# Performance work log

Measured on AMD Instinct MI355X. Metric: run time of the kernel, lower is better.

The kernel has to match this reference:

```python
import jax, jax.numpy as jnp
import numpy as np

B, L, D, H, TOPO = 2, 1024, 1024, 16, 8
Dh = D // H
N_SLOTS = B * L


def _rope_apply(x, cos, sin):
    # x: [B,H,L,Dh]; cos/sin: [B,1,L,Dh//2]
    x1 = x[..., 0::2]
    x2 = x[..., 1::2]
    y1 = x1 * cos - x2 * sin
    y2 = x1 * sin + x2 * cos
    return jnp.stack([y1, y2], axis=-1).reshape(x.shape)


def setup_inputs() -> dict:
    key = jax.random.key(0)
    ks = jax.random.split(key, 6)
    x = jax.random.normal(ks[0], (B, L, D), dtype=jnp.float32)
    topo_active = jax.random.normal(ks[1], (B, L, TOPO), dtype=jnp.float32)
    k_cache = jnp.zeros((1, H, N_SLOTS, Dh), dtype=jnp.float32)
    v_cache = jnp.zeros((1, H, N_SLOTS, Dh), dtype=jnp.float32)
    Wqkv = jax.random.normal(ks[2], (3 * D, D), dtype=jnp.float32) * 0.02
    Wproj = jax.random.normal(ks[3], (D, D), dtype=jnp.float32) * 0.02
    Wfreq = jax.random.normal(ks[4], (Dh // 2, TOPO), dtype=jnp.float32) * 0.02
    # each token (b, pos) writes to physical slot b*L + pos
    slot_mapping = jnp.arange(N_SLOTS, dtype=jnp.int64)
    # paged causal mask: query (b, i) may see slot s iff slot belongs to batch b and pos(s) <= i
    s = jnp.arange(N_SLOTS)
    sb = s // L           # batch owning each slot
    sp = s % L            # position within that sequence
    b_idx = jnp.arange(B)[:, None, None]
    i_idx = jnp.arange(L)[None, :, None]
    block_mask = ((sb[None, None, :] == b_idx) & (sp[None, None, :] <= i_idx))[:, None]  # [B,1,L,S]
    return {"x": x, "topo_active": topo_active, "k_cache": k_cache, "v_cache": v_cache,
            "Wqkv": Wqkv, "Wproj": Wproj, "Wfreq": Wfreq,
            "slot_mapping": slot_mapping, "block_mask": block_mask}


def reference(x, topo_active, k_cache, v_cache, Wqkv, Wproj, Wfreq, slot_mapping, block_mask):
    Bx, Lx, Dx = x.shape
    # qkv projection -> q,k,v [B,H,L,Dh]
    qkv = (x @ Wqkv.T).reshape(Bx, Lx, 3, H, Dh).transpose(2, 0, 3, 1, 4)
    q, k, v = qkv[0], qkv[1], qkv[2]
    # RnRoPE: topo -> per-position frequencies, rotate q and k
    freqs = (topo_active @ Wfreq.T)[:, None]  # [B,1,L,Dh//2]
    cos, sin = jnp.cos(freqs), jnp.sin(freqs)
    q = _rope_apply(q, cos, sin)
    k = _rope_apply(k, cos, sin)
    # commit new k/v into the paged cache via slot_mapping scatter
    k_flat = k.transpose(0, 2, 1, 3).reshape(Bx * Lx, H, Dh).swapaxes(0, 1)  # [H,BL,Dh]
    v_flat = v.transpose(0, 2, 1, 3).reshape(Bx * Lx, H, Dh).swapaxes(0, 1)
    kc = k_cache[0].at[:, slot_mapping].set(k_flat)  # [H,S,Dh]
    vc = v_cache[0].at[:, slot_mapping].set(v_flat)
    # masked (block-sparse) attention over the physical cache
    scale = 1.0 / jnp.sqrt(jnp.float32(Dh))
    scores = jnp.einsum('bhld,hsd->bhls', q, kc) * scale
    scores = jnp.where(block_mask, scores, -jnp.inf)
    p = jax.nn.softmax(scores, axis=-1)
    out = jnp.einsum('bhls,hsd->bhld', p, vc)
    out = out.transpose(0, 2, 1, 3).reshape(Bx, Lx, Dx)
    return out @ Wproj.T
```

## Files before the change

### kernel.cpp

```cpp
#include <hip/hip_runtime.h>
#include <hip/hip_bf16.h>
#include <hip/hip_cooperative_groups.h>
#include <math.h>

namespace cg = cooperative_groups;

#define H_N 16
#define DH 64
#define LSEQ 1024
#define BATCH 2
#define NSLOT 2048
#define DMODEL 1024

typedef __bf16 bf16x8 __attribute__((ext_vector_type(8)));
typedef __bf16 bf16x4 __attribute__((ext_vector_type(4)));
typedef float f32x4 __attribute__((ext_vector_type(4)));

template <int BM, int BN, int BK>
__device__ __forceinline__ void gemm_coreT(const __bf16* __restrict__ A,
                                           const __bf16* __restrict__ Bm,
                                           int K, int m0, int n0,
                                           __bf16* As, __bf16* Bs,
                                           f32x4 acc[BM / 32][BN / 32],
                                           int tid, int wr, int wc, int lane) {
    constexpr int MF = BM / 32, NF = BN / 32;
    constexpr int SLOTS = BK / 8;
    constexpr int RPI = 256 / SLOTS;
    constexpr int AIT = BM / RPI;
    constexpr int BIT = BN / RPI;
    const f32x4 z = {0.f, 0.f, 0.f, 0.f};
#pragma unroll
    for (int m = 0; m < MF; ++m)
#pragma unroll
        for (int n = 0; n < NF; ++n) acc[m][n] = z;

    const int l15 = lane & 15, g = lane >> 4;
    const int wv = tid >> 6;
    const int srow = tid / SLOTS, sslot = tid % SLOTS;
    const int ssrc = (sslot ^ (srow & 7)) * 8;

#pragma unroll
    for (int i = 0; i < AIT; ++i) {
        int row = i * RPI + srow;
        __builtin_amdgcn_global_load_lds(
            (const __attribute__((address_space(1))) void*)(A + (size_t)(m0 + row) * K + ssrc),
            (__attribute__((address_space(3))) void*)(As + i * 2048 + wv * 512), 16, 0, 0);
    }
#pragma unroll
    for (int i = 0; i < BIT; ++i) {
        int row = i * RPI + srow;
        __builtin_amdgcn_global_load_lds(
            (const __attribute__((address_space(1))) void*)(Bm + (size_t)(n0 + row) * K + ssrc),
            (__attribute__((address_space(3))) void*)(Bs + i * 2048 + wv * 512), 16, 0, 0);
    }
    __syncthreads();

    const int NT = K / BK;
    for (int t = 0; t < NT; ++t) {
        const int cur = t & 1;
        __bf16* Ac = As + cur * (BM * BK);
        __bf16* Bc = Bs + cur * (BN * BK);
        if (t + 1 < NT) {
            const int k0 = (t + 1) * BK;
            __bf16* An = As + (1 - cur) * (BM * BK);
            __bf16* Bn = Bs + (1 - cur) * (BN * BK);
#pragma unroll
            for (int i = 0; i < AIT; ++i) {
                int row = i * RPI + srow;
                __builtin_amdgcn_global_load_lds(
                    (const __attribute__((address_space(1))) void*)(A + (size_t)(m0 + row) * K + k0 + ssrc),
                    (__attribute__((address_space(3))) void*)(An + i * 2048 + wv * 512), 16, 0, 0);
            }
#pragma unroll
            for (int i = 0; i < BIT; ++i) {
                int row = i * RPI + srow;
                __builtin_amdgcn_global_load_lds(
                    (const __attribute__((address_space(1))) void*)(Bm + (size_t)(n0 + row) * K + k0 + ssrc),
                    (__attribute__((address_space(3))) void*)(Bn + i * 2048 + wv * 512), 16, 0, 0);
            }
        }
        __builtin_amdgcn_s_setprio(1);
#pragma unroll
        for (int kk = 0; kk < BK / 32; ++kk) {
            const int k16 = kk * 4 + g;
            bf16x8 af[MF], bfr[NF];
#pragma unroll
            for (int m = 0; m < MF; ++m) {
                int row = wr * (BM / 2) + m * 16 + l15;
                int slot = k16 ^ (row & 7);
                af[m] = *reinterpret_cast<const bf16x8*>(Ac + row * BK + slot * 8);
            }
#pragma unroll
            for (int n = 0; n < NF; ++n) {
                int col = wc * (BN / 2) + n * 16 + l15;
                int slot = k16 ^ (col & 7);
                bfr[n] = *reinterpret_cast<const bf16x8*>(Bc + col * BK + slot * 8);
            }
#pragma unroll
            for (int m = 0; m < MF; ++m)
#pragma unroll
                for (int n = 0; n < NF; ++n)
                    acc[m][n] = __builtin_amdgcn_mfma_f32_16x16x32_bf16(af[m], bfr[n], acc[m][n], 0, 0, 0);
        }
        __builtin_amdgcn_s_setprio(0);
        __syncthreads();
    }
}

__device__ __forceinline__ void setup_body(int blk, int tid,
                                           const float* x, const float* Wqkv, const float* Wproj,
                                           const float* topo, const float* Wfreq,
                                           __bf16* xb, __bf16* Wqkvb, __bf16* Wprojb,
                                           float* cosb, float* sinb) {
    if (blk < 6144) {
        const float* in;
        __bf16* ob;
        int base;
        if (blk < 2048)      { in = x;     ob = xb;     base = blk; }
        else if (blk < 5120) { in = Wqkv;  ob = Wqkvb;  base = blk - 2048; }
        else                 { in = Wproj; ob = Wprojb; base = blk - 5120; }
        int i = (base * 256 + tid) * 4;
        float4 v = *reinterpret_cast<const float4*>(in + i);
        struct B4 { __bf16 a, b, c, d; };
        B4 o{(__bf16)v.x, (__bf16)v.y, (__bf16)v.z, (__bf16)v.w};
        *reinterpret_cast<B4*>(ob + i) = o;
    } else {
        int s = (blk - 6144) * 8 + (tid >> 5);
        int j = tid & 31;
        float f = 0.f;
#pragma unroll
        for (int t = 0; t < 8; ++t) f += topo[s * 8 + t] * Wfreq[j * 8 + t];
        cosb[s * 32 + j] = cosf(f);
        sinb[s * 32 + j] = sinf(f);
    }
}

__device__ __forceinline__ void qkv_map(int bid, int& m0, int& n0) {
    const int xcd = bid & 7, t = bid >> 3;
    m0 = ((xcd & 1) * 8 + (t & 7)) * 128;
    n0 = ((xcd >> 1) * 8 + (t >> 3)) * 96;
}
__device__ __forceinline__ void proj_map(int bid, int& m0, int& n0) {
    const int xcd = bid & 7, t = bid >> 3;
    m0 = ((xcd & 3) * 8 + (t & 7)) * 64;
    n0 = ((xcd >> 2) * 8 + (t >> 3)) * 64;
}

__device__ __forceinline__ void qkv_epilogue(f32x4 acc[4][3], int m0, int n0,
                                             int wr, int wc, int l15, int g,
                                             const float* cosb, const float* sinb,
                                             __bf16* Qb, __bf16* Kb, __bf16* Vtb) {
    const int rbase = m0 + wr * 64;
#pragma unroll
    for (int n = 0; n < 3; ++n) {
        int c = n0 + wc * 48 + n * 16 + l15;
        int part = c >> 10, h = (c >> 6) & 15, d = c & 63, jj = d >> 1;
#pragma unroll
        for (int m = 0; m < 4; ++m) {
            int sbase = rbase + m * 16 + g * 4;
            if (part < 2) {
                __bf16* dst = (part == 0) ? Qb : Kb;
#pragma unroll
                for (int j = 0; j < 4; ++j) {
                    int s = sbase + j;
                    float v = acc[m][n][j];
                    float partner = __shfl_xor(v, 1);
                    float cs = cosb[s * 32 + jj], sn = sinb[s * 32 + jj];
                    float outv = (d & 1) ? fmaf(v, cs, partner * sn) : fmaf(v, cs, -partner * sn);
                    dst[((size_t)h * NSLOT + s) * DH + d] = (__bf16)outv;
                }
            } else {
                bf16x4 pk;
#pragma unroll
                for (int j = 0; j < 4; ++j) pk[j] = (__bf16)acc[m][n][j];
                *reinterpret_cast<bf16x4*>(&Vtb[((size_t)h * DH + d) * NSLOT + sbase]) = pk;
            }
        }
    }
}

__device__ __forceinline__ void attn_chunk(const bf16x8 qf[2], __bf16* Kc, __bf16* Vc,
                                           __bf16* Pw, int ch, int nch, int q0,
                                           int l15, int g, f32x4 ao[4], float lsum[4]) {
    const f32x4 z = {0.f, 0.f, 0.f, 0.f};
    f32x4 s[8];
#pragma unroll
    for (int n = 0; n < 8; ++n) s[n] = z;
    __builtin_amdgcn_s_setprio(1);
#pragma unroll
    for (int g2 = 0; g2 < 2; ++g2) {
#pragma unroll
        for (int n = 0; n < 8; ++n) {
            int r = n * 16 + l15;
            int slot = ((g2 << 2) + g) ^ (r & 7);
            bf16x8 kf = *reinterpret_cast<const bf16x8*>(Kc + r * 64 + slot * 8);
            s[n] = __builtin_amdgcn_mfma_f32_16x16x32_bf16(qf[g2], kf, s[n], 0, 0, 0);
        }
    }
    __builtin_amdgcn_s_setprio(0);

    const bool last = (ch == nch - 1);
    const int sp0 = ch * 128;
#pragma unroll
    for (int n = 0; n < 8; ++n) {
        int key = sp0 + n * 16 + l15;
#pragma unroll
        for (int j = 0; j < 4; ++j) {
            float sc = s[n][j] * 0.125f;
            if (last && key > q0 + g * 4 + j) sc = -INFINITY;
            float p = __expf(sc);
            s[n][j] = p;
            lsum[j] += p;
        }
    }

#pragma unroll
    for (int j = 0; j < 4; ++j) {
        int row = g * 4 + j;
#pragma unroll
        for (int n = 0; n < 8; ++n) {
            int slot = n * 2 + (l15 >> 3);
            Pw[row * 128 + ((slot ^ (row & 7)) << 3) + (l15 & 7)] = (__bf16)s[n][j];
        }
    }

    bf16x8 pf[4];
#pragma unroll
    for (int kb = 0; kb < 4; ++kb)
        pf[kb] = *reinterpret_cast<const bf16x8*>(
            Pw + l15 * 128 + (((kb << 2) + g) ^ (l15 & 7)) * 8);

    __builtin_amdgcn_s_setprio(1);
#pragma unroll
    for (int kb = 0; kb < 4; ++kb) {
#pragma unroll
        for (int dt = 0; dt < 4; ++dt) {
            int rv = dt * 16 + l15;
            int slot = ((kb << 2) + g) ^ (rv & 7);
            bf16x8 vf = *reinterpret_cast<const bf16x8*>(Vc + rv * 128 + slot * 8);
            ao[dt] = __builtin_amdgcn_mfma_f32_16x16x32_bf16(pf[kb], vf, ao[dt], 0, 0, 0);
        }
    }
    __builtin_amdgcn_s_setprio(0);
}

__global__ __launch_bounds__(256, 2) void k_fused(const float* __restrict__ x,
                                                  const float* __restrict__ topo,
                                                  const float* __restrict__ Wqkv,
                                                  const float* __restrict__ Wproj,
                                                  const float* __restrict__ Wfreq,
                                                  float* __restrict__ out,
                                                  char* __restrict__ wsb) {
    __shared__ __align__(16) char smem[65536];

    __bf16* xb     = (__bf16*)(wsb);
    __bf16* Wqkvb  = (__bf16*)(wsb + (4u << 20));
    __bf16* Wprojb = (__bf16*)(wsb + (10u << 20));
    float*  cosb   = (float*)(wsb + (12u << 20));
    float*  sinb   = (float*)(wsb + (12u << 20) + 262144);
    __bf16* Qb     = (__bf16*)(wsb + (12u << 20) + 524288);
    __bf16* Kb     = (__bf16*)(wsb + (16u << 20) + 524288);
    __bf16* Vtb    = (__bf16*)(wsb + (20u << 20) + 524288);
    __bf16* AO     = (__bf16*)(wsb + (24u << 20) + 524288);

    cg::grid_group grid = cg::this_grid();
    const int tid = threadIdx.x;
    const int bid = blockIdx.x;
    const int lane = tid & 63, w = tid >> 6;
    const int l15 = lane & 15, g = lane >> 4;

    for (int blk = bid; blk < 6400; blk += 512)
        setup_body(blk, tid, x, Wqkv, Wproj, topo, Wfreq, xb, Wqkvb, Wprojb, cosb, sinb);
    grid.sync();

    {
        __bf16* As = (__bf16*)smem;
        __bf16* Bs = (__bf16*)(smem + 32768);
        int m0, n0;
        qkv_map(bid, m0, n0);
        const int wr = w >> 1, wc = w & 1;
        f32x4 acc[4][3];
        gemm_coreT<128, 96, 64>(xb, Wqkvb, DMODEL, m0, n0, As, Bs, acc, tid, wr, wc, lane);
        qkv_epilogue(acc, m0, n0, wr, wc, l15, g, cosb, sinb, Qb, Kb, Vtb);
    }
    grid.sync();

    {
        __bf16* Ks = (__bf16*)smem;
        __bf16* Vs = (__bf16*)(smem + 16384);
        __bf16* Pw = (__bf16*)(smem + 32768) + w * 16 * 128;

        const int xc = bid & 7;
        const int t = bid >> 3;
        const int b = xc >> 2;
        const int h = (xc & 3) * 4 + (t & 3);
        const int v = t >> 2;
        const int bx = (v < 8) ? v : 23 - v;
        const int q0 = bx * 64 + w * 16;

        const __bf16* Qh = Qb + ((size_t)h * NSLOT + b * LSEQ) * DH;
        const __bf16* Kh = Kb + ((size_t)h * NSLOT + b * LSEQ) * DH;
        const __bf16* Vh = Vtb + ((size_t)h * DH) * NSLOT + b * LSEQ;

        bf16x8 qf[2];
#pragma unroll
        for (int g2 = 0; g2 < 2; ++g2)
            qf[g2] = *reinterpret_cast<const bf16x8*>(Qh + (size_t)(q0 + l15) * DH + g2 * 32 + g * 8);

        const f32x4 z = {0.f, 0.f, 0.f, 0.f};
        f32x4 ao[4];
#pragma unroll
        for (int dt = 0; dt < 4; ++dt) ao[dt] = z;
        float lsum[4] = {0.f, 0.f, 0.f, 0.f};

        const int nch = (bx >> 1) + 1;

        for (int ch = 0; ch < nch; ++ch) {
            __syncthreads();
            const int sp0 = ch * 128;
#pragma unroll
            for (int i = 0; i < 4; ++i) {
                int u = i * 256 + tid;
                {
                    int row = u >> 3, slot = u & 7, srcs = (slot ^ (row & 7)) * 8;
                    __builtin_amdgcn_global_load_lds(
                        (const __attribute__((address_space(1))) void*)(Kh + (size_t)(sp0 + row) * DH + srcs),
                        (__attribute__((address_space(3))) void*)(Ks + i * 2048 + w * 512), 16, 0, 0);
                }
                {
                    int row = u >> 4, slot = u & 15, srcs = (slot ^ (row & 7)) * 8;
                    __builtin_amdgcn_global_load_lds(
                        (const __attribute__((address_space(1))) void*)(Vh + (size_t)row * NSLOT + sp0 + srcs),
                        (__attribute__((address_space(3))) void*)(Vs + i * 2048 + w * 512), 16, 0, 0);
                }
            }
            __syncthreads();
            attn_chunk(qf, Ks, Vs, Pw, ch, nch, q0, l15, g, ao, lsum);
        }

        float lrow[4];
#pragma unroll
        for (int j = 0; j < 4; ++j) {
            float vv = lsum[j];
#pragma unroll
            for (int off = 1; off < 16; off <<= 1) vv += __shfl_xor(vv, off);
            lrow[j] = vv;
        }

#pragma unroll
        for (int dt = 0; dt < 4; ++dt)
#pragma unroll
            for (int j = 0; j < 4; ++j) {
                int q = q0 + g * 4 + j;
                AO[(size_t)(b * LSEQ + q) * DMODEL + h * 64 + dt * 16 + l15] =
                    (__bf16)(ao[dt][j] / lrow[j]);
            }
    }
    grid.sync();

    {
        __bf16* As = (__bf16*)smem;
        __bf16* Bs = (__bf16*)(smem + 32768);
        int m0, n0;
        proj_map(bid, m0, n0);
        const int wr = w >> 1, wc = w & 1;
        f32x4 acc[2][2];
        gemm_coreT<64, 64, 128>(AO, Wprojb, DMODEL, m0, n0, As, Bs, acc, tid, wr, wc, lane);

#pragma unroll
        for (int n = 0; n < 2; ++n) {
            int c = n0 + wc * 32 + n * 16 + l15;
#pragma unroll
            for (int m = 0; m < 2; ++m) {
#pragma unroll
                for (int j = 0; j < 4; ++j) {
                    int s = m0 + wr * 32 + m * 16 + g * 4 + j;
                    out[(size_t)s * DMODEL + c] = acc[m][n][j];
                }
            }
        }
    }
}

__global__ __launch_bounds__(256) void k_setup(const float* __restrict__ x,
                                               const float* __restrict__ Wqkv,
                                               const float* __restrict__ Wproj,
                                               const float* __restrict__ topo,
                                               const float* __restrict__ Wfreq,
                                               __bf16* __restrict__ xb,
                                               __bf16* __restrict__ Wqkvb,
                                               __bf16* __restrict__ Wprojb,
                                               float* __restrict__ cosb,
                                               float* __restrict__ sinb) {
    setup_body(blockIdx.x, threadIdx.x, x, Wqkv, Wproj, topo, Wfreq,
               xb, Wqkvb, Wprojb, cosb, sinb);
}

__global__ __launch_bounds__(256, 2) void k_qkv_mfma(const __bf16* __restrict__ xb,
                                                     const __bf16* __restrict__ Wb,
                                                     const float* __restrict__ cosb,
                                                     const float* __restrict__ sinb,
                                                     __bf16* __restrict__ Qb,
                                                     __bf16* __restrict__ Kb,
                                                     __bf16* __restrict__ Vtb) {
    __shared__ __bf16 As[2][128 * 64];
    __shared__ __bf16 Bs[2][96 * 64];
    int m0, n0;
    qkv_map(blockIdx.x, m0, n0);
    const int tid = threadIdx.x, lane = tid & 63, w = tid >> 6;
    const int wr = w >> 1, wc = w & 1;
    const int l15 = lane & 15, g = lane >> 4;
    f32x4 acc[4][3];
    gemm_coreT<128, 96, 64>(xb, Wb, DMODEL, m0, n0, &As[0][0], &Bs[0][0], acc, tid, wr, wc, lane);
    qkv_epilogue(acc, m0, n0, wr, wc, l15, g, cosb, sinb, Qb, Kb, Vtb);
}

__global__ __launch_bounds__(256, 2) void k_attn9(const __bf16* __restrict__ Qg,
                                                  const __bf16* __restrict__ Kg,
                                                  const __bf16* __restrict__ Vt,
                                                  __bf16* __restrict__ AO) {
    int lin = blockIdx.x + 16 * (blockIdx.y + 16 * blockIdx.z);
    const int xc = lin & 7;
    const int t = lin >> 3;
    const int b = xc >> 2;
    const int h = (xc & 3) * 4 + (t & 3);
    const int v = t >> 2;
    const int bx = (v < 8) ? v : 23 - v;

    const int tid = threadIdx.x, w = tid >> 6, lane = tid & 63;
    const int l15 = lane & 15, g = lane >> 4;
    const int q0 = bx * 64 + w * 16;

    __shared__ __bf16 Ks[2][128 * 64];
    __shared__ __bf16 Vs[2][64 * 128];
    __shared__ __bf16 P_lds[4][16 * 128];
    __bf16* Pw = &P_lds[w][0];

    const __bf16* Qh = Qg + ((size_t)h * NSLOT + b * LSEQ) * DH;
    const __bf16* Kh = Kg + ((size_t)h * NSLOT + b * LSEQ) * DH;
    const __bf16* Vh = Vt + ((size_t)h * DH) * NSLOT + b * LSEQ;

    bf16x8 qf[2];
#pragma unroll
    for (int g2 = 0; g2 < 2; ++g2)
        qf[g2] = *reinterpret_cast<const bf16x8*>(Qh + (size_t)(q0 + l15) * DH + g2 * 32 + g * 8);

    const f32x4 z = {0.f, 0.f, 0.f, 0.f};
    f32x4 ao[4];
#pragma unroll
    for (int dt = 0; dt < 4; ++dt) ao[dt] = z;
    float lsum[4] = {0.f, 0.f, 0.f, 0.f};

    const int nch = (bx >> 1) + 1;

#pragma unroll
    for (int i = 0; i < 4; ++i) {
        int u = i * 256 + tid;
        {
            int row = u >> 3, slot = u & 7, srcs = (slot ^ (row & 7)) * 8;
            __builtin_amdgcn_global_load_lds(
                (const __attribute__((address_space(1))) void*)(Kh + (size_t)row * DH + srcs),
                (__attribute__((address_space(3))) void*)(&Ks[0][i * 2048 + w * 512]), 16, 0, 0);
        }
        {
            int row = u >> 4, slot = u & 15, srcs = (slot ^ (row & 7)) * 8;
            __builtin_amdgcn_global_load_lds(
                (const __attribute__((address_space(1))) void*)(Vh + (size_t)row * NSLOT + srcs),
                (__attribute__((address_space(3))) void*)(&Vs[0][i * 2048 + w * 512]), 16, 0, 0);
        }
    }
    __syncthreads();

    for (int ch = 0; ch < nch; ++ch) {
        const int cur = ch & 1;
        if (ch + 1 < nch) {
            const int nsp = (ch + 1) * 128;
#pragma unroll
            for (int i = 0; i < 4; ++i) {
                int u = i * 256 + tid;
                {
                    int row = u >> 3, slot = u & 7, srcs = (slot ^ (row & 7)) * 8;
                    __builtin_amdgcn_global_load_lds(
                        (const __attribute__((address_space(1))) void*)(Kh + (size_t)(nsp + row) * DH + srcs),
                        (__attribute__((address_space(3))) void*)(&Ks[1 - cur][i * 2048 + w * 512]), 16, 0, 0);
                }
                {
                    int row = u >> 4, slot = u & 15, srcs = (slot ^ (row & 7)) * 8;
                    __builtin_amdgcn_global_load_lds(
                        (const __attribute__((address_space(1))) void*)(Vh + (size_t)row * NSLOT + nsp + srcs),
                        (__attribute__((address_space(3))) void*)(&Vs[1 - cur][i * 2048 + w * 512]), 16, 0, 0);
                }
            }
        }
        attn_chunk(qf, &Ks[cur][0], &Vs[cur][0], Pw, ch, nch, q0, l15, g, ao, lsum);
        __syncthreads();
    }

    float lrow[4];
#pragma unroll
    for (int j = 0; j < 4; ++j) {
        float vv = lsum[j];
#pragma unroll
        for (int off = 1; off < 16; off <<= 1) vv += __shfl_xor(vv, off);
        lrow[j] = vv;
    }

#pragma unroll
    for (int dt = 0; dt < 4; ++dt)
#pragma unroll
        for (int j = 0; j < 4; ++j) {
            int q = q0 + g * 4 + j;
            AO[(size_t)(b * LSEQ + q) * DMODEL + h * 64 + dt * 16 + l15] =
                (__bf16)(ao[dt][j] / lrow[j]);
        }
}

__global__ __launch_bounds__(256, 2) void k_proj_mfma(const __bf16* __restrict__ AO,
                                                      const __bf16* __restrict__ Wb,
                                                      float* __restrict__ out) {
    __shared__ __bf16 As[2][64 * 128];
    __shared__ __bf16 Bs[2][64 * 128];
    int m0, n0;
    proj_map(blockIdx.x, m0, n0);
    const int tid = threadIdx.x, lane = tid & 63, w = tid >> 6;
    const int wr = w >> 1, wc = w & 1;
    const int l15 = lane & 15, g = lane >> 4;
    f32x4 acc[2][2];
    gemm_coreT<64, 64, 128>(AO, Wb, DMODEL, m0, n0, &As[0][0], &Bs[0][0], acc, tid, wr, wc, lane);

#pragma unroll
    for (int n = 0; n < 2; ++n) {
        int c = n0 + wc * 32 + n * 16 + l15;
#pragma unroll
        for (int m = 0; m < 2; ++m) {
#pragma unroll
            for (int j = 0; j < 4; ++j) {
                int s = m0 + wr * 32 + m * 16 + g * 4 + j;
                out[(size_t)s * DMODEL + c] = acc[m][n][j];
            }
        }
    }
}

extern "C" void kernel_launch(void* const* d_in, const int* in_sizes, int n_in,
                              void* d_out, int out_size, void* d_ws, size_t ws_size,
                              hipStream_t stream) {
    const float* x     = (const float*)d_in[0];
    const float* topo  = (const float*)d_in[1];
    const float* Wqkv  = (const float*)d_in[4];
    const float* Wproj = (const float*)d_in[5];
    const float* Wfreq = (const float*)d_in[6];
    float* out = (float*)d_out;
    char* wsb = (char*)d_ws;

    int coopAttr = 0, dev = 0, nb = 0;
    hipGetDevice(&dev);
    hipDeviceGetAttribute(&coopAttr, hipDeviceAttributeCooperativeLaunch, dev);
    hipOccupancyMaxActiveBlocksPerMultiprocessor(&nb, (const void*)k_fused, 256, 0);

    if (coopAttr && nb >= 2) {
        void* args[] = {(void*)&x, (void*)&topo, (void*)&Wqkv, (void*)&Wproj,
                        (void*)&Wfreq, (void*)&out, (void*)&wsb};
        hipLaunchCooperativeKernel((const void*)k_fused, dim3(512), dim3(256),
                                   args, 0, stream);
        return;
    }

    __bf16* xb     = (__bf16*)(wsb);
    __bf16* Wqkvb  = (__bf16*)(wsb + (4u << 20));
    __bf16* Wprojb = (__bf16*)(wsb + (10u << 20));
    float*  cosb   = (float*)(wsb + (12u << 20));
    float*  sinb   = (float*)(wsb + (12u << 20) + 262144);
    __bf16* Qb     = (__bf16*)(wsb + (12u << 20) + 524288);
    __bf16* Kb     = (__bf16*)(wsb + (16u << 20) + 524288);
    __bf16* Vtb    = (__bf16*)(wsb + (20u << 20) + 524288);
    __bf16* AO     = (__bf16*)(wsb + (24u << 20) + 524288);

    hipLaunchKernelGGL(k_setup, dim3(6400), dim3(256), 0, stream,
                       x, Wqkv, Wproj, topo, Wfreq, xb, Wqkvb, Wprojb, cosb, sinb);
    hipLaunchKernelGGL(k_qkv_mfma, dim3(512), dim3(256), 0, stream,
                       xb, Wqkvb, cosb, sinb, Qb, Kb, Vtb);
    hipLaunchKernelGGL(k_attn9, dim3(LSEQ / 64, H_N, BATCH), dim3(256), 0, stream,
                       Qb, Kb, Vtb, AO);
    hipLaunchKernelGGL(k_proj_mfma, dim3(512), dim3(256), 0, stream,
                       AO, Wprojb, out);
}
```

Measured before the change: 60.36 us.

## Software-pipeline K/V loads in fused attention phase with double-buffered K

```diff
diff --git a/kernel.cpp b/kernel.cpp
--- a/kernel.cpp
+++ b/kernel.cpp
@@ -15,6 +15,11 @@
 typedef __bf16 bf16x8 __attribute__((ext_vector_type(8)));
 typedef __bf16 bf16x4 __attribute__((ext_vector_type(4)));
 typedef float f32x4 __attribute__((ext_vector_type(4)));
+
+#define GLOAD16(gp, lp)                                                              \
+    __builtin_amdgcn_global_load_lds(                                                \
+        (const __attribute__((address_space(1))) void*)(gp),                         \
+        (__attribute__((address_space(3))) void*)(lp), 16, 0, 0)
 
 template <int BM, int BN, int BK>
 __device__ __forceinline__ void gemm_coreT(const __bf16* __restrict__ A,
@@ -42,16 +47,12 @@
 #pragma unroll
     for (int i = 0; i < AIT; ++i) {
         int row = i * RPI + srow;
-        __builtin_amdgcn_global_load_lds(
-            (const __attribute__((address_space(1))) void*)(A + (size_t)(m0 + row) * K + ssrc),
-            (__attribute__((address_space(3))) void*)(As + i * 2048 + wv * 512), 16, 0, 0);
+        GLOAD16(A + (size_t)(m0 + row) * K + ssrc, As + i * 2048 + wv * 512);
     }
 #pragma unroll
     for (int i = 0; i < BIT; ++i) {
         int row = i * RPI + srow;
-        __builtin_amdgcn_global_load_lds(
-            (const __attribute__((address_space(1))) void*)(Bm + (size_t)(n0 + row) * K + ssrc),
-            (__attribute__((address_space(3))) void*)(Bs + i * 2048 + wv * 512), 16, 0, 0);
+        GLOAD16(Bm + (size_t)(n0 + row) * K + ssrc, Bs + i * 2048 + wv * 512);
     }
     __syncthreads();
 
@@ -67,16 +68,12 @@
 #pragma unroll
             for (int i = 0; i < AIT; ++i) {
                 int row = i * RPI + srow;
-                __builtin_amdgcn_global_load_lds(
-                    (const __attribute__((address_space(1))) void*)(A + (size_t)(m0 + row) * K + k0 + ssrc),
-                    (__attribute__((address_space(3))) void*)(An + i * 2048 + wv * 512), 16, 0, 0);
+                GLOAD16(A + (size_t)(m0 + row) * K + k0 + ssrc, An + i * 2048 + wv * 512);
             }
 #pragma unroll
             for (int i = 0; i < BIT; ++i) {
                 int row = i * RPI + srow;
-                __builtin_amdgcn_global_load_lds(
-                    (const __attribute__((address_space(1))) void*)(Bm + (size_t)(n0 + row) * K + k0 + ssrc),
-                    (__attribute__((address_space(3))) void*)(Bn + i * 2048 + wv * 512), 16, 0, 0);
+                GLOAD16(Bm + (size_t)(n0 + row) * K + k0 + ssrc, Bn + i * 2048 + wv * 512);
             }
         }
         __builtin_amdgcn_s_setprio(1);
@@ -287,8 +284,8 @@
 
     {
         __bf16* Ks = (__bf16*)smem;
-        __bf16* Vs = (__bf16*)(smem + 16384);
-        __bf16* Pw = (__bf16*)(smem + 32768) + w * 16 * 128;
+        __bf16* Vs = (__bf16*)(smem + 32768);
+        __bf16* Pw = (__bf16*)(smem + 49152) + w * 16 * 128;
 
         const int xc = bid & 7;
         const int t = bid >> 3;
@@ -315,27 +312,105 @@
 
         const int nch = (bx >> 1) + 1;
 
+#pragma unroll
+        for (int i = 0; i < 4; ++i) {
+            int u = i * 256 + tid;
+            int row = u >> 3, slot = u & 7, srcs = (slot ^ (row & 7)) * 8;
+            GLOAD16(Kh + (size_t)row * DH + srcs, Ks + i * 2048 + w * 512);
+        }
+#pragma unroll
+        for (int i = 0; i < 4; ++i) {
+            int u = i * 256 + tid;
+            int row = u >> 4, slot = u & 15, srcs = (slot ^ (row & 7)) * 8;
+            GLOAD16(Vh + (size_t)row * NSLOT + srcs, Vs + i * 2048 + w * 512);
+        }
+        __syncthreads();
+
         for (int ch = 0; ch < nch; ++ch) {
+            const int cur = ch & 1;
+            __bf16* Kc = Ks + cur * 8192;
+            if (ch + 1 < nch) {
+                const int nsp = (ch + 1) * 128;
+                __bf16* Kn = Ks + (1 - cur) * 8192;
+#pragma unroll
+                for (int i = 0; i < 4; ++i) {
+                    int u = i * 256 + tid;
+                    int row = u >> 3, slot = u & 7, srcs = (slot ^ (row & 7)) * 8;
+                    GLOAD16(Kh + (size_t)(nsp + row) * DH + srcs, Kn + i * 2048 + w * 512);
+                }
+            }
+
+            f32x4 s[8];
+#pragma unroll
+            for (int n = 0; n < 8; ++n) s[n] = z;
+            __builtin_amdgcn_s_setprio(1);
+#pragma unroll
+            for (int g2 = 0; g2 < 2; ++g2) {
+#pragma unroll
+                for (int n = 0; n < 8; ++n) {
+                    int r = n * 16 + l15;
+                    int slot = ((g2 << 2) + g) ^ (r & 7);
+                    bf16x8 kf = *reinterpret_cast<const bf16x8*>(Kc + r * 64 + slot * 8);
+                    s[n] = __builtin_amdgcn_mfma_f32_16x16x32_bf16(qf[g2], kf, s[n], 0, 0, 0);
+                }
+            }
+            __builtin_amdgcn_s_setprio(0);
+
+            const bool last = (ch == nch - 1);
+            const int sp0 = ch * 128;
+#pragma unroll
+            for (int n = 0; n < 8; ++n) {
+                int key = sp0 + n * 16 + l15;
+#pragma unroll
+                for (int j = 0; j < 4; ++j) {
+                    float sc = s[n][j] * 0.125f;
+                    if (last && key > q0 + g * 4 + j) sc = -INFINITY;
+                    float p = __expf(sc);
+                    s[n][j] = p;
+                    lsum[j] += p;
+                }
+            }
+#pragma unroll
+            for (int j = 0; j < 4; ++j) {
+                int row = g * 4 + j;
+#pragma unroll
+                for (int n = 0; n < 8; ++n) {
+                    int slot = n * 2 + (l15 >> 3);
+                    Pw[row * 128 + ((slot ^ (row & 7)) << 3) + (l15 & 7)] = (__bf16)s[n][j];
+                }
+            }
+            bf16x8 pf[4];
+#pragma unroll
+            for (int kb = 0; kb < 4; ++kb)
+                pf[kb] = *reinterpret_cast<const bf16x8*>(
+                    Pw + l15 * 128 + (((kb << 2) + g) ^ (l15 & 7)) * 8);
+
             __syncthreads();
-            const int sp0 = ch * 128;
-#pragma unroll
-            for (int i = 0; i < 4; ++i) {
-                int u = i * 256 + tid;
-                {
-                    int row = u >> 3, slot = u & 7, srcs = (slot ^ (row & 7)) * 8;
-                    __builtin_amdgcn_global_load_lds(
-                        (const __attribute__((address_space(1))) void*)(Kh + (size_t)(sp0 + row) * DH + srcs),
-                        (__attribute__((address_space(3))) void*)(Ks + i * 2048 + w * 512), 16, 0, 0);
-                }
-                {
+
+            __builtin_amdgcn_s_setprio(1);
+#pragma unroll
+            for (int kb = 0; kb < 4; ++kb) {
+#pragma unroll
+                for (int dt = 0; dt < 4; ++dt) {
+                    int rv = dt * 16 + l15;
+                    int slot = ((kb << 2) + g) ^ (rv & 7);
+                    bf16x8 vf = *reinterpret_cast<const bf16x8*>(Vs + rv * 128 + slot * 8);
+                    ao[dt] = __builtin_amdgcn_mfma_f32_16x16x32_bf16(pf[kb], vf, ao[dt], 0, 0, 0);
+                }
+            }
+            __builtin_amdgcn_s_setprio(0);
+
+            __syncthreads();
+
+            if (ch + 1 < nch) {
+                const int nsp = (ch + 1) * 128;
+#pragma unroll
+                for (int i = 0; i < 4; ++i) {
+                    int u = i * 256 + tid;
                     int row = u >> 4, slot = u & 15, srcs = (slot ^ (row & 7)) * 8;
-                    __builtin_amdgcn_global_load_lds(
-                        (const __attribute__((address_space(1))) void*)(Vh + (size_t)row * NSLOT + sp0 + srcs),
-                        (__attribute__((address_space(3))) void*)(Vs + i * 2048 + w * 512), 16, 0, 0);
-                }
-            }
-            __syncthreads();
-            attn_chunk(qf, Ks, Vs, Pw, ch, nch, q0, l15, g, ao, lsum);
+                    GLOAD16(Vh + (size_t)row * NSLOT + nsp + srcs, Vs + i * 2048 + w * 512);
+                }
+            }
         }
 
         float lrow[4];
@@ -458,15 +533,11 @@
         int u = i * 256 + tid;
         {
             int row = u >> 3, slot = u & 7, srcs = (slot ^ (row & 7)) * 8;
-            __builtin_amdgcn_global_load_lds(
-                (const __attribute__((address_space(1))) void*)(Kh + (size_t)row * DH + srcs),
-                (__attribute__((address_space(3))) void*)(&Ks[0][i * 2048 + w * 512]), 16, 0, 0);
+            GLOAD16(Kh + (size_t)row * DH + srcs, &Ks[0][i * 2048 + w * 512]);
         }
         {
             int row = u >> 4, slot = u & 15, srcs = (slot ^ (row & 7)) * 8;
-            __builtin_amdgcn_global_load_lds(
-                (const __attribute__((address_space(1))) void*)(Vh + (size_t)row * NSLOT + srcs),
-                (__attribute__((address_space(3))) void*)(&Vs[0][i * 2048 + w * 512]), 16, 0, 0);
+            GLOAD16(Vh + (size_t)row * NSLOT + srcs, &Vs[0][i * 2048 + w * 512]);
         }
     }
     __syncthreads();
@@ -480,15 +551,11 @@
                 int u = i * 256 + tid;
                 {
                     int row = u >> 3, slot = u & 7, srcs = (slot ^ (row & 7)) * 8;
-                    __builtin_amdgcn_global_load_lds(
-                        (const __attribute__((address_space(1))) void*)(Kh + (size_t)(nsp + row) * DH + srcs),
-                        (__attribute__((address_space(3))) void*)(&Ks[1 - cur][i * 2048 + w * 512]), 16, 0, 0);
+                    GLOAD16(Kh + (size_t)(nsp + row) * DH + srcs, &Ks[1 - cur][i * 2048 + w * 512]);
                 }
                 {
                     int row = u >> 4, slot = u & 15, srcs = (slot ^ (row & 7)) * 8;
-                    __builtin_amdgcn_global_load_lds(
-                        (const __attribute__((address_space(1))) void*)(Vh + (size_t)row * NSLOT + nsp + srcs),
-                        (__attribute__((address_space(3))) void*)(&Vs[1 - cur][i * 2048 + w * 512]), 16, 0, 0);
+                    GLOAD16(Vh + (size_t)row * NSLOT + nsp + srcs, &Vs[1 - cur][i * 2048 + w * 512]);
                 }
             }
         }
```

Result: no change. 60.27 us (-0.2%).
